# Performance work log

Hardware: AMD Instinct MI355X
Metric: run time of the kernel (lower is better)

## Reference

```python
import jax, jax.numpy as jnp
import numpy as np

B, L, H, S, EXP = 8, 2048, 256, 64, 2
E = H * EXP

def setup_inputs() -> dict:
    key = jax.random.key(0)
    ks = jax.random.split(key, 12)
    u = jax.random.normal(ks[0], (B, L, H), dtype=jnp.float32)
    W_in = jax.random.normal(ks[1], (H, 2 * E), dtype=jnp.float32) * 0.02
    b_in = jax.random.normal(ks[2], (2 * E,), dtype=jnp.float32) * 0.02
    conv_w = jax.random.normal(ks[3], (E, 3), dtype=jnp.float32) * 0.3  # depthwise k=3
    conv_b = jax.random.normal(ks[4], (E,), dtype=jnp.float32) * 0.02
    W_x = jax.random.normal(ks[5], (E, 3 * S), dtype=jnp.float32) * 0.02
    b_x = jax.random.normal(ks[6], (3 * S,), dtype=jnp.float32) * 0.02
    A_log = jax.random.normal(ks[7], (S,), dtype=jnp.float32) * 0.1
    Dp = jnp.ones((E,), dtype=jnp.float32)
    W_out = jax.random.normal(ks[8], (E, H), dtype=jnp.float32) * 0.02
    b_out = jax.random.normal(ks[9], (H,), dtype=jnp.float32) * 0.02
    ln_g = jnp.ones((E,), dtype=jnp.float32)
    ln_b = jnp.zeros((E,), dtype=jnp.float32)
    return {"u": u, "W_in": W_in, "b_in": b_in, "conv_w": conv_w, "conv_b": conv_b,
            "W_x": W_x, "b_x": b_x, "A_log": A_log, "Dp": Dp,
            "W_out": W_out, "b_out": b_out, "ln_g": ln_g, "ln_b": ln_b}

def reference(u, W_in, b_in, conv_w, conv_b, W_x, b_x, A_log, Dp, W_out, b_out, ln_g, ln_b):
    Bb, Ll, Hh = u.shape
    Ss = A_log.shape[0]
    Ee = Dp.shape[0]
    xz = u @ W_in + b_in                      # [B,L,2E]
    x, z = jnp.split(xz, 2, axis=-1)          # [B,L,E] each
    # depthwise conv1d, kernel=3, padding=1 along L
    xp = jnp.pad(x, ((0, 0), (1, 1), (0, 0)))
    x = xp[:, :-2] * conv_w[:, 0] + xp[:, 1:-1] * conv_w[:, 1] + xp[:, 2:] * conv_w[:, 2] + conv_b
    x = jax.nn.silu(x)
    ssm = x @ W_x + b_x                       # [B,L,3S]
    delta, Bm, Cm = jnp.split(ssm, 3, axis=-1)
    delta = jax.nn.softplus(delta)            # [B,L,S]
    A = -jnp.exp(jnp.clip(A_log, -5.0, 5.0))  # [S]
    # torch broadcast quirk: delta[...,None] * A[None,None,:] -> [B,L,S,S], entry = delta[b,l,i]*A[j]
    A_d = jnp.exp(jnp.clip(delta[:, :, :, None] * A[None, None, None, :], -10.0, 0.0))  # [B,L,S,S]
    # bmm(B_discrete, x[:,t,:,None]) == (delta*B) * sum_e x, broadcast over E
    inp_term = (delta * Bm) * x.sum(-1, keepdims=True)  # [B,L,S]

    def step(h, inputs):
        A_t, it_t, C_t, x_t = inputs          # [B,S,S],[B,S],[B,S],[B,E]
        h = jnp.einsum('bij,bje->bie', A_t, h) + it_t[:, :, None]
        h = jnp.clip(h, -100.0, 100.0)
        y = jnp.einsum('bse,bs->be', h, C_t) + Dp * x_t
        return h, y

    h0 = jnp.zeros((Bb, Ss, Ee), dtype=u.dtype)
    xs = (jnp.swapaxes(A_d, 0, 1), jnp.swapaxes(inp_term, 0, 1),
          jnp.swapaxes(Cm, 0, 1), jnp.swapaxes(x, 0, 1))
    _, ys = jax.lax.scan(step, h0, xs)
    outputs = jnp.swapaxes(ys, 0, 1)          # [B,L,E]
    mu = outputs.mean(-1, keepdims=True)
    var = ((outputs - mu) ** 2).mean(-1, keepdims=True)
    y = (outputs - mu) / jnp.sqrt(var + 1e-5) * ln_g + ln_b
    y = y * jax.nn.silu(z)
    return y @ W_out + b_out  # dropout is identity in eval mode
```

## Files before the change

kernel.cpp:

```cpp
#include <hip/hip_runtime.h>
#include <hip/hip_bf16.h>

constexpr int BB = 8;
constexpr int LLEN = 2048;
constexpr int HH = 256;
constexpr int EE = 512;
constexpr int MM = BB * LLEN;

typedef short bf16x8 __attribute__((ext_vector_type(8)));
typedef float f32x4  __attribute__((ext_vector_type(4)));

static __device__ inline unsigned short f2bf(float f) {
    unsigned u = __builtin_bit_cast(unsigned, f);
    unsigned r = (u + 0x7FFFu + ((u >> 16) & 1u)) >> 16;
    return (unsigned short)r;
}
static __device__ inline float bf2f(unsigned short h) {
    return __builtin_bit_cast(float, (unsigned)h << 16);
}

#define GL2LDS(gp, lp) __builtin_amdgcn_global_load_lds( \
    (const __attribute__((address_space(1))) void*)(gp), \
    (__attribute__((address_space(3))) void*)(lp), 16, 0, 0)

__global__ __launch_bounds__(256) void cast_bf16_kernel(
    const float* __restrict__ in, unsigned short* __restrict__ out)
{
    int i = (blockIdx.x * 256 + threadIdx.x) * 4;
    float4 v = *reinterpret_cast<const float4*>(in + i);
    ushort4 o = {f2bf(v.x), f2bf(v.y), f2bf(v.z), f2bf(v.w)};
    *reinterpret_cast<ushort4*>(out + i) = o;
}

__global__ __launch_bounds__(256) void transpose_cast_kernel(
    const float* __restrict__ W, unsigned short* __restrict__ Wt, int K, int N)
{
    int i = blockIdx.x * 256 + threadIdx.x;
    if (i < K * N) {
        int n = i / K, k = i - n * K;
        Wt[i] = f2bf(W[(size_t)k * N + n]);
    }
}

template<int K, bool BF16OUT, bool SILU1>
__global__ __launch_bounds__(256) void gemm_bf16_mfma(
    const unsigned short* __restrict__ A, const unsigned short* __restrict__ Bt,
    const float* __restrict__ bias, void* __restrict__ C0v, void* __restrict__ C1v,
    int split, int ldc0, int ldc1)
{
    __shared__ unsigned short Al[128 * 32];
    __shared__ unsigned short Bl[128 * 32];

    const int tid = threadIdx.x;
    const int lane = tid & 63;
    const int wave = tid >> 6;
    const int wrow = wave >> 1, wcol = wave & 1;
    const int row0 = blockIdx.y * 128;
    const int col0 = blockIdx.x * 128;

    const int l15 = lane & 15;
    const int lk  = lane >> 4;
    const int swz = (l15 >> 1) & 3;
    const int aoff = (wrow * 64 + l15) * 32 + ((lk ^ swz) << 3);
    const int boff = (wcol * 64 + l15) * 32 + ((lk ^ swz) << 3);

    f32x4 acc[4][4] = {};

    for (int kt = 0; kt < K; kt += 32) {
        #pragma unroll
        for (int q = 0; q < 2; ++q) {
            int id = q * 256 + tid;
            int r = id >> 2, s = id & 3;
            int ksw = kt + (((s ^ ((r >> 1) & 3)) << 3));
            GL2LDS(A + (size_t)(row0 + r) * K + ksw, &Al[id * 8]);
        }
        #pragma unroll
        for (int q = 0; q < 2; ++q) {
            int id = q * 256 + tid;
            int r = id >> 2, s = id & 3;
            int ksw = kt + (((s ^ ((r >> 1) & 3)) << 3));
            GL2LDS(Bt + (size_t)(col0 + r) * K + ksw, &Bl[id * 8]);
        }
        __syncthreads();

        bf16x8 af[4], bfr[4];
        #pragma unroll
        for (int m = 0; m < 4; ++m)
            af[m] = *reinterpret_cast<const bf16x8*>(&Al[aoff + m * 512]);
        #pragma unroll
        for (int n = 0; n < 4; ++n)
            bfr[n] = *reinterpret_cast<const bf16x8*>(&Bl[boff + n * 512]);
        #pragma unroll
        for (int m = 0; m < 4; ++m)
            #pragma unroll
            for (int n = 0; n < 4; ++n)
                acc[m][n] = __builtin_amdgcn_mfma_f32_16x16x32_bf16(
                    af[m], bfr[n], acc[m][n], 0, 0, 0);
        __syncthreads();
    }

    #pragma unroll
    for (int m = 0; m < 4; ++m) {
        #pragma unroll
        for (int n = 0; n < 4; ++n) {
            int col = col0 + wcol * 64 + n * 16 + l15;
            float bv = bias[col];
            #pragma unroll
            for (int i = 0; i < 4; ++i) {
                int row = row0 + wrow * 64 + m * 16 + lk * 4 + i;
                float v = acc[m][n][i] + bv;
                if (col < split) {
                    if (BF16OUT)
                        ((unsigned short*)C0v)[(size_t)row * ldc0 + col] = f2bf(v);
                    else
                        ((float*)C0v)[(size_t)row * ldc0 + col] = v;
                } else {
                    float w = SILU1 ? (v / (1.f + __expf(-v))) : v;
                    if (BF16OUT)
                        ((unsigned short*)C1v)[(size_t)row * ldc1 + (col - split)] = f2bf(w);
                    else
                        ((float*)C1v)[(size_t)row * ldc1 + (col - split)] = w;
                }
            }
        }
    }
}

__global__ __launch_bounds__(256) void mid_kernel(
    const unsigned short* __restrict__ x, const unsigned short* __restrict__ zs,
    unsigned short* __restrict__ g,
    const float* __restrict__ conv_w, const float* __restrict__ conv_b,
    const float* __restrict__ Dp, const float* __restrict__ ln_g,
    const float* __restrict__ ln_b)
{
    const int lane = threadIdx.x & 63;
    const int wid  = threadIdx.x >> 6;
    const int row  = blockIdx.x * 4 + wid;
    const int l    = row & (LLEN - 1);
    const int e0   = lane * 8;
    const size_t base = (size_t)row * EE + e0;

    bf16x8 xc = *reinterpret_cast<const bf16x8*>(x + base);
    bf16x8 xm = {}, xp = {};
    if (l > 0)        xm = *reinterpret_cast<const bf16x8*>(x + base - EE);
    if (l < LLEN - 1) xp = *reinterpret_cast<const bf16x8*>(x + base + EE);

    float o[8];
    float s1 = 0.f, s2 = 0.f;
    #pragma unroll
    for (int j = 0; j < 8; ++j) {
        int e = e0 + j;
        float v = conv_b[e]
                + bf2f((unsigned short)xm[j]) * conv_w[e * 3 + 0]
                + bf2f((unsigned short)xc[j]) * conv_w[e * 3 + 1]
                + bf2f((unsigned short)xp[j]) * conv_w[e * 3 + 2];
        float sx = v / (1.f + __expf(-v));
        float oe = Dp[e] * sx;
        o[j] = oe;
        s1 += oe;
        s2 += oe * oe;
    }

    #pragma unroll
    for (int off = 1; off < 64; off <<= 1) {
        s1 += __shfl_xor(s1, off);
        s2 += __shfl_xor(s2, off);
    }

    const float mu  = s1 * (1.f / EE);
    const float var = s2 * (1.f / EE) - mu * mu;
    const float inv = rsqrtf(var + 1e-5f);

    bf16x8 zv = *reinterpret_cast<const bf16x8*>(zs + base);
    bf16x8 ov;
    #pragma unroll
    for (int j = 0; j < 8; ++j) {
        int e = e0 + j;
        float gy = ((o[j] - mu) * inv * ln_g[e] + ln_b[e]) * bf2f((unsigned short)zv[j]);
        ov[j] = (short)f2bf(gy);
    }
    *reinterpret_cast<bf16x8*>(g + base) = ov;
}

extern "C" void kernel_launch(void* const* d_in, const int* in_sizes, int n_in,
                              void* d_out, int out_size, void* d_ws, size_t ws_size,
                              hipStream_t stream)
{
    const float* u      = (const float*)d_in[0];
    const float* W_in   = (const float*)d_in[1];
    const float* b_in   = (const float*)d_in[2];
    const float* conv_w = (const float*)d_in[3];
    const float* conv_b = (const float*)d_in[4];
    const float* Dp     = (const float*)d_in[8];
    const float* W_out  = (const float*)d_in[9];
    const float* b_out  = (const float*)d_in[10];
    const float* ln_g   = (const float*)d_in[11];
    const float* ln_b   = (const float*)d_in[12];
    float* out = (float*)d_out;

    char* ws = (char*)d_ws;
    unsigned short* ubf   = (unsigned short*)ws; ws += (size_t)MM * HH * 2;
    unsigned short* wtin  = (unsigned short*)ws; ws += (size_t)1024 * HH * 2;
    unsigned short* wtout = (unsigned short*)ws; ws += (size_t)HH * EE * 2;
    unsigned short* xbuf  = (unsigned short*)ws; ws += (size_t)MM * EE * 2;
    unsigned short* zsbuf = (unsigned short*)ws; ws += (size_t)MM * EE * 2;
    unsigned short* gbuf  = (unsigned short*)ws;

    dim3 blk(256);

    cast_bf16_kernel<<<dim3(MM * HH / 1024), blk, 0, stream>>>(u, ubf);
    transpose_cast_kernel<<<dim3((1024 * HH + 255) / 256), blk, 0, stream>>>(W_in, wtin, HH, 1024);
    transpose_cast_kernel<<<dim3((HH * EE + 255) / 256), blk, 0, stream>>>(W_out, wtout, EE, HH);

    gemm_bf16_mfma<HH, true, true><<<dim3(1024 / 128, MM / 128), blk, 0, stream>>>(
        ubf, wtin, b_in, xbuf, zsbuf, EE, EE, EE);

    mid_kernel<<<dim3(MM / 4), blk, 0, stream>>>(
        xbuf, zsbuf, gbuf, conv_w, conv_b, Dp, ln_g, ln_b);

    gemm_bf16_mfma<EE, false, false><<<dim3(HH / 128, MM / 128), blk, 0, stream>>>(
        gbuf, wtout, b_out, out, out, 1 << 30, HH, HH);
}
```

Before: 72.04 us.

## Double-buffer GEMM LDS tiles with BK=64 and remap blocks across XCDs

Replaces the GEMM kernel with a templated version that uses BK=64, double-buffered LDS staging, explicit vmcnt waits and a barrier-based pipeline so the next tile's global loads overlap the current MFMA work. It switches to an XOR swizzle over 8 slots and uses a 128x64 tile for the output GEMM so more blocks run. The cast, mid and GEMM kernels also remap block indices so consecutive tiles land on the same XCD, aiming for better L2 locality. This doubles LDS use per block and ties correctness to grid sizes that are divisible by 8.

Result: faster. 62.54 us (-13.2%).

```diff
diff --git a/kernel.cpp b/kernel.cpp
--- a/kernel.cpp
+++ b/kernel.cpp
@@ -26,7 +26,10 @@
 __global__ __launch_bounds__(256) void cast_bf16_kernel(
     const float* __restrict__ in, unsigned short* __restrict__ out)
 {
-    int i = (blockIdx.x * 256 + threadIdx.x) * 4;
+    int b = blockIdx.x;
+    int cpx = gridDim.x >> 3;
+    int lin = (b & 7) * cpx + (b >> 3);
+    int i = (lin * 256 + threadIdx.x) * 4;
     float4 v = *reinterpret_cast<const float4*>(in + i);
     ushort4 o = {f2bf(v.x), f2bf(v.y), f2bf(v.z), f2bf(v.w)};
     *reinterpret_cast<ushort4*>(out + i) = o;
@@ -42,72 +45,108 @@
     }
 }
 
-template<int K, bool BF16OUT, bool SILU1>
-__global__ __launch_bounds__(256) void gemm_bf16_mfma(
+template<int BM, int BN, int K, int MFR, int NFR, int GX, bool BF16OUT, bool SILU1>
+__global__ __launch_bounds__(256) void gemm2(
     const unsigned short* __restrict__ A, const unsigned short* __restrict__ Bt,
     const float* __restrict__ bias, void* __restrict__ C0v, void* __restrict__ C1v,
     int split, int ldc0, int ldc1)
 {
-    __shared__ unsigned short Al[128 * 32];
-    __shared__ unsigned short Bl[128 * 32];
+    constexpr int BK = 64;
+    constexpr int NT = K / BK;
+    constexpr int AL = BM * 8 / 256;
+    constexpr int BL = BN * 8 / 256;
+    constexpr int NL = AL + BL;
+    constexpr int WCOLS = BN / (16 * NFR);
+
+    __shared__ unsigned short Al[2][BM * BK];
+    __shared__ unsigned short Bl[2][BN * BK];
 
     const int tid = threadIdx.x;
     const int lane = tid & 63;
     const int wave = tid >> 6;
-    const int wrow = wave >> 1, wcol = wave & 1;
-    const int row0 = blockIdx.y * 128;
-    const int col0 = blockIdx.x * 128;
-
+    const int wrow = wave / WCOLS, wcol = wave % WCOLS;
     const int l15 = lane & 15;
     const int lk  = lane >> 4;
-    const int swz = (l15 >> 1) & 3;
-    const int aoff = (wrow * 64 + l15) * 32 + ((lk ^ swz) << 3);
-    const int boff = (wcol * 64 + l15) * 32 + ((lk ^ swz) << 3);
-
-    f32x4 acc[4][4] = {};
-
-    for (int kt = 0; kt < K; kt += 32) {
-        #pragma unroll
-        for (int q = 0; q < 2; ++q) {
-            int id = q * 256 + tid;
-            int r = id >> 2, s = id & 3;
-            int ksw = kt + (((s ^ ((r >> 1) & 3)) << 3));
-            GL2LDS(A + (size_t)(row0 + r) * K + ksw, &Al[id * 8]);
-        }
-        #pragma unroll
-        for (int q = 0; q < 2; ++q) {
-            int id = q * 256 + tid;
-            int r = id >> 2, s = id & 3;
-            int ksw = kt + (((s ^ ((r >> 1) & 3)) << 3));
-            GL2LDS(Bt + (size_t)(col0 + r) * K + ksw, &Bl[id * 8]);
-        }
-        __syncthreads();
-
-        bf16x8 af[4], bfr[4];
-        #pragma unroll
-        for (int m = 0; m < 4; ++m)
-            af[m] = *reinterpret_cast<const bf16x8*>(&Al[aoff + m * 512]);
-        #pragma unroll
-        for (int n = 0; n < 4; ++n)
-            bfr[n] = *reinterpret_cast<const bf16x8*>(&Bl[boff + n * 512]);
-        #pragma unroll
-        for (int m = 0; m < 4; ++m)
-            #pragma unroll
-            for (int n = 0; n < 4; ++n)
-                acc[m][n] = __builtin_amdgcn_mfma_f32_16x16x32_bf16(
-                    af[m], bfr[n], acc[m][n], 0, 0, 0);
-        __syncthreads();
-    }
-
-    #pragma unroll
-    for (int m = 0; m < 4; ++m) {
-        #pragma unroll
-        for (int n = 0; n < 4; ++n) {
-            int col = col0 + wcol * 64 + n * 16 + l15;
+
+    const int cpx = gridDim.x >> 3;
+    int lin = blockIdx.x;
+    lin = (lin & 7) * cpx + (lin >> 3);
+    const int row0 = (lin / GX) * BM;
+    const int col0 = (lin % GX) * BN;
+
+    f32x4 acc[MFR][NFR] = {};
+
+    auto stage = [&](int bi, int kt) {
+        const unsigned short* Ab = A + (size_t)row0 * K + kt;
+        #pragma unroll
+        for (int i = 0; i < AL; ++i) {
+            int sid = i * 256 + tid;
+            int r = sid >> 3, sl = sid & 7;
+            GL2LDS(Ab + (size_t)r * K + ((sl ^ (r & 7)) << 3), &Al[bi][sid * 8]);
+        }
+        const unsigned short* Bb = Bt + (size_t)col0 * K + kt;
+        #pragma unroll
+        for (int i = 0; i < BL; ++i) {
+            int sid = i * 256 + tid;
+            int r = sid >> 3, sl = sid & 7;
+            GL2LDS(Bb + (size_t)r * K + ((sl ^ (r & 7)) << 3), &Bl[bi][sid * 8]);
+        }
+    };
+
+    stage(0, 0);
+
+    #pragma unroll
+    for (int t = 0; t < NT; ++t) {
+        const int bi = t & 1;
+        if (t + 1 < NT) {
+            stage(bi ^ 1, (t + 1) * BK);
+            asm volatile("s_waitcnt vmcnt(%0)" :: "n"(NL) : "memory");
+        } else {
+            asm volatile("s_waitcnt vmcnt(0)" ::: "memory");
+        }
+        __builtin_amdgcn_sched_barrier(0);
+        __builtin_amdgcn_s_barrier();
+
+        bf16x8 af[MFR][2], bfr[NFR][2];
+        #pragma unroll
+        for (int m = 0; m < MFR; ++m) {
+            const int r = wrow * (MFR * 16) + m * 16 + l15;
+            #pragma unroll
+            for (int kk = 0; kk < 2; ++kk) {
+                const int sl = (kk * 4 + lk) ^ (r & 7);
+                af[m][kk] = *reinterpret_cast<const bf16x8*>(&Al[bi][r * 64 + sl * 8]);
+            }
+        }
+        #pragma unroll
+        for (int n = 0; n < NFR; ++n) {
+            const int r = wcol * (NFR * 16) + n * 16 + l15;
+            #pragma unroll
+            for (int kk = 0; kk < 2; ++kk) {
+                const int sl = (kk * 4 + lk) ^ (r & 7);
+                bfr[n][kk] = *reinterpret_cast<const bf16x8*>(&Bl[bi][r * 64 + sl * 8]);
+            }
+        }
+        #pragma unroll
+        for (int kk = 0; kk < 2; ++kk)
+            #pragma unroll
+            for (int m = 0; m < MFR; ++m)
+                #pragma unroll
+                for (int n = 0; n < NFR; ++n)
+                    acc[m][n] = __builtin_amdgcn_mfma_f32_16x16x32_bf16(
+                        af[m][kk], bfr[n][kk], acc[m][n], 0, 0, 0);
+
+        __builtin_amdgcn_s_barrier();
+    }
+
+    #pragma unroll
+    for (int m = 0; m < MFR; ++m) {
+        #pragma unroll
+        for (int n = 0; n < NFR; ++n) {
+            int col = col0 + wcol * (NFR * 16) + n * 16 + l15;
             float bv = bias[col];
             #pragma unroll
             for (int i = 0; i < 4; ++i) {
-                int row = row0 + wrow * 64 + m * 16 + lk * 4 + i;
+                int row = row0 + wrow * (MFR * 16) + m * 16 + lk * 4 + i;
                 float v = acc[m][n][i] + bv;
                 if (col < split) {
                     if (BF16OUT)
@@ -135,7 +174,10 @@
 {
     const int lane = threadIdx.x & 63;
     const int wid  = threadIdx.x >> 6;
-    const int row  = blockIdx.x * 4 + wid;
+    int b = blockIdx.x;
+    int cpx = gridDim.x >> 3;
+    int lin = (b & 7) * cpx + (b >> 3);
+    const int row  = lin * 4 + wid;
     const int l    = row & (LLEN - 1);
     const int e0   = lane * 8;
     const size_t base = (size_t)row * EE + e0;
@@ -212,12 +254,12 @@
     transpose_cast_kernel<<<dim3((1024 * HH + 255) / 256), blk, 0, stream>>>(W_in, wtin, HH, 1024);
     transpose_cast_kernel<<<dim3((HH * EE + 255) / 256), blk, 0, stream>>>(W_out, wtout, EE, HH);
 
-    gemm_bf16_mfma<HH, true, true><<<dim3(1024 / 128, MM / 128), blk, 0, stream>>>(
+    gemm2<128, 128, HH, 4, 4, 8, true, true><<<dim3(1024), blk, 0, stream>>>(
         ubf, wtin, b_in, xbuf, zsbuf, EE, EE, EE);
 
     mid_kernel<<<dim3(MM / 4), blk, 0, stream>>>(
         xbuf, zsbuf, gbuf, conv_w, conv_b, Dp, ln_g, ln_b);
 
-    gemm_bf16_mfma<EE, false, false><<<dim3(HH / 128, MM / 128), blk, 0, stream>>>(
+    gemm2<128, 64, EE, 4, 2, 4, false, false><<<dim3(512), blk, 0, stream>>>(
         gbuf, wtout, b_out, out, out, 1 << 30, HH, HH);
 }
```
